# Kernel optimization log

Hardware: AMD Instinct MI355X
Metric: run time of the kernel (lower is better)

## Reference

```python
import jax, jax.numpy as jnp
import numpy as np

BATCH, D_IN, D_OUT = 2048, 1024, 4096


def setup_inputs() -> dict:
    key = jax.random.key(0)
    kx, kw = jax.random.split(key)
    x = jax.random.normal(kx, (BATCH, D_IN), dtype=jnp.float32)
    W = jax.random.normal(kw, (D_IN, D_OUT), dtype=jnp.float32)  # nn.Parameter init: N(0,1)
    return {"x": x, "W": W}


def reference(x, W):
    # out[b,o] = -1/2 * sum_i (x[b,i] - W[i,o])^2
    # instead of materializing the [B, O, I] broadcast tensor.
    x_sq = jnp.sum(x * x, axis=1, keepdims=True)          # [B, 1]
    w_sq = jnp.sum(W * W, axis=0, keepdims=True)          # [1, O]
    xw = jnp.matmul(x, W)                                  # [B, O] GEMM
    return -0.5 * (x_sq - 2.0 * xw + w_sq)
```

## Files before the change

### kernel.cpp

```cpp
#include <hip/hip_runtime.h>
#include <stdint.h>

#define BATCH 2048
#define DIN   1024
#define DOUT  4096


__device__ __forceinline__ ushort f2bf(float f) {
    uint32_t u = __float_as_uint(f);
    u += 0x7fffu + ((u >> 16) & 1u);
    return (ushort)(u >> 16);
}

__device__ __forceinline__ void async_copy16(const void* gsrc, void* ldst) {
    __builtin_amdgcn_global_load_lds(
        reinterpret_cast<uint32_t __attribute__((address_space(1)))*>(
            reinterpret_cast<uintptr_t>(gsrc)),
        reinterpret_cast<uint32_t __attribute__((address_space(3)))*>(
            reinterpret_cast<uintptr_t>(ldst)),
        16, 0, 0);
}

typedef __bf16 bf16x8 __attribute__((ext_vector_type(8)));
typedef float  f32x4  __attribute__((ext_vector_type(4)));

__global__ __launch_bounds__(256) void prep_fused(
    const float* __restrict__ x, const float* __restrict__ W,
    ushort* __restrict__ xb, ushort* __restrict__ wbt,
    float* __restrict__ xsq, float* __restrict__ wsq_part)
{
    __shared__ float smem[64 * 65 + 64];
    const int t = threadIdx.x;

    if (blockIdx.x < BATCH) {
        const int row = blockIdx.x;
        const float4 v = *(const float4*)(x + (size_t)row * DIN + t * 4);
        ushort4 pk;
        pk.x = f2bf(v.x); pk.y = f2bf(v.y); pk.z = f2bf(v.z); pk.w = f2bf(v.w);
        *(ushort4*)(xb + (size_t)row * DIN + t * 4) = pk;

        float s = v.x * v.x + v.y * v.y + v.z * v.z + v.w * v.w;
        #pragma unroll
        for (int off = 32; off > 0; off >>= 1) s += __shfl_down(s, off);
        if ((t & 63) == 0) smem[t >> 6] = s;
        __syncthreads();
        if (t == 0) xsq[row] = smem[0] + smem[1] + smem[2] + smem[3];
    } else {
        const int wblk = blockIdx.x - BATCH;
        const int o0 = (wblk & 63) * 64;
        const int i0 = (wblk >> 6) * 64;
        float (*tile)[65] = (float(*)[65])smem;
        float* csum = smem + 64 * 65;
        const int c4 = (t & 15) * 4;
        const int r0 = t >> 4;

        if (t < 64) csum[t] = 0.f;
        __syncthreads();

        float ss0 = 0.f, ss1 = 0.f, ss2 = 0.f, ss3 = 0.f;
        #pragma unroll
        for (int p = 0; p < 4; ++p) {
            const int r = r0 + p * 16;
            const float4 v = *(const float4*)&W[(size_t)(i0 + r) * DOUT + o0 + c4];
            tile[r][c4 + 0] = v.x; tile[r][c4 + 1] = v.y;
            tile[r][c4 + 2] = v.z; tile[r][c4 + 3] = v.w;
            ss0 += v.x * v.x; ss1 += v.y * v.y;
            ss2 += v.z * v.z; ss3 += v.w * v.w;
        }
        atomicAdd(&csum[c4 + 0], ss0);
        atomicAdd(&csum[c4 + 1], ss1);
        atomicAdd(&csum[c4 + 2], ss2);
        atomicAdd(&csum[c4 + 3], ss3);
        __syncthreads();
        if (t < 64) wsq_part[(size_t)(wblk >> 6) * DOUT + o0 + t] = csum[t];

        #pragma unroll
        for (int p = 0; p < 4; ++p) {
            const int orow = r0 + p * 16;
            ushort4 pk;
            pk.x = f2bf(tile[c4 + 0][orow]);
            pk.y = f2bf(tile[c4 + 1][orow]);
            pk.z = f2bf(tile[c4 + 2][orow]);
            pk.w = f2bf(tile[c4 + 3][orow]);
            *(ushort4*)&wbt[(size_t)(o0 + orow) * DIN + i0 + c4] = pk;
        }
    }
}

#define BM 128
#define BN 128
#define BK 64
#define NT (DIN / BK)

__global__ __launch_bounds__(256, 2) void gemm_epi(
    const ushort* __restrict__ A,
    const ushort* __restrict__ Bt,
    const float* __restrict__ xsq,
    const float* __restrict__ wsq_part,
    float* __restrict__ out)
{
    __shared__ __align__(16) ushort sA[2][BM * BK];
    __shared__ __align__(16) ushort sB[2][BN * BK];

    const int tid  = threadIdx.x;
    const int wv   = tid >> 6;
    const int lane = tid & 63;
    const int wr = wv >> 1, wc = wv & 1;

    const int bid = blockIdx.x;
    const int k = bid & 7, loc = bid >> 3;
    const int bx = (k & 3) * 8 + (loc & 7);
    const int by = (k >> 2) * 8 + (loc >> 3);
    const int m0 = by * BM;
    const int n0 = bx * BN;

    const int srow = tid >> 3;
    const int scol = (((tid & 7) ^ (srow & 7)) << 3);
    const ushort* ag = A  + (size_t)(m0 + srow) * DIN + scol;
    const ushort* bg = Bt + (size_t)(n0 + srow) * DIN + scol;

    const int fr  = lane & 15;
    const int q4  = lane >> 4;
    const int x7  = lane & 7;
    const int arow = wr * 64 + fr;
    const int brow = wc * 64 + fr;
    const int sl0 = ((q4)     ^ x7) << 3;
    const int sl1 = ((4 + q4) ^ x7) << 3;

    f32x4 acc[4][4] = {};

    auto stage = [&](int b, int kt) {
        ushort* da = &sA[b][0] + wv * 512;
        ushort* db = &sB[b][0] + wv * 512;
        #pragma unroll
        for (int q = 0; q < 4; ++q) {
            async_copy16(ag + (size_t)q * 32 * DIN + kt, da + q * 2048);
            async_copy16(bg + (size_t)q * 32 * DIN + kt, db + q * 2048);
        }
    };

    stage(0, 0);
    __syncthreads();
    int cur = 0;

    for (int t = 0; t < NT; ++t) {
        if (t + 1 < NT) stage(cur ^ 1, (t + 1) * BK);

        const ushort* pa = &sA[cur][0];
        const ushort* pb = &sB[cur][0];
        bf16x8 fa[2][4], fb[2][4];
        #pragma unroll
        for (int i = 0; i < 4; ++i) {
            fa[0][i] = *(const bf16x8*)&pa[(arow + i * 16) * BK + sl0];
            fa[1][i] = *(const bf16x8*)&pa[(arow + i * 16) * BK + sl1];
            fb[0][i] = *(const bf16x8*)&pb[(brow + i * 16) * BK + sl0];
            fb[1][i] = *(const bf16x8*)&pb[(brow + i * 16) * BK + sl1];
        }

        __builtin_amdgcn_s_setprio(1);
        #pragma unroll
        for (int ks = 0; ks < 2; ++ks)
            #pragma unroll
            for (int mi = 0; mi < 4; ++mi)
                #pragma unroll
                for (int ni = 0; ni < 4; ++ni)
                    acc[mi][ni] = __builtin_amdgcn_mfma_f32_16x16x32_bf16(
                        fa[ks][mi], fb[ks][ni], acc[mi][ni], 0, 0, 0);
        __builtin_amdgcn_s_setprio(0);

        __syncthreads();
        cur ^= 1;
    }

    const int er = q4 * 4;
    const int ec = fr;

    float wt[4];
    #pragma unroll
    for (int ni = 0; ni < 4; ++ni) {
        const int col = n0 + wc * 64 + ni * 16 + ec;
        float s = 0.f;
        #pragma unroll
        for (int j = 0; j < 16; ++j) s += wsq_part[(size_t)j * DOUT + col];
        wt[ni] = s;
    }

    #pragma unroll
    for (int mi = 0; mi < 4; ++mi) {
        const int row = m0 + wr * 64 + mi * 16 + er;
        #pragma unroll
        for (int ni = 0; ni < 4; ++ni) {
            const int col = n0 + wc * 64 + ni * 16 + ec;
            #pragma unroll
            for (int r = 0; r < 4; ++r) {
                out[(size_t)(row + r) * DOUT + col] =
                    acc[mi][ni][r] - 0.5f * (xsq[row + r] + wt[ni]);
            }
        }
    }
}


extern "C" void kernel_launch(void* const* d_in, const int* in_sizes, int n_in,
                              void* d_out, int out_size, void* d_ws, size_t ws_size,
                              hipStream_t stream) {
    const float* x = (const float*)d_in[0];
    const float* W = (const float*)d_in[1];
    float* out = (float*)d_out;

    char* ws = (char*)d_ws;
    ushort* xb  = (ushort*)ws;
    ushort* wbt = (ushort*)(ws + (4u << 20));
    float*  xsq = (float*)(ws + (12u << 20));
    float*  wsq_part = (float*)(ws + (12u << 20) + (16u << 10));

    prep_fused<<<BATCH + (DOUT / 64) * (DIN / 64), 256, 0, stream>>>(
        x, W, xb, wbt, xsq, wsq_part);
    gemm_epi<<<(DOUT / BN) * (BATCH / BM), 256, 0, stream>>>(
        xb, wbt, xsq, wsq_part, out);
}
```

Before: 105.0 us.

## Fuse prep and GEMM into one persistent kernel with a grid barrier

Merges the bf16 conversion/norm prep kernel and the GEMM-epilogue kernel into a single launch. Each of the 512 blocks processes six prep units, then all blocks synchronize through a global atomic counter before running the GEMM, with LDS shared via a union. This aims to remove the inter-kernel launch gap, but it adds a memset launch and a spin barrier that relies on all blocks being co-resident.

```diff
diff --git a/kernel.cpp b/kernel.cpp
--- a/kernel.cpp
+++ b/kernel.cpp
@@ -24,90 +24,98 @@
 typedef __bf16 bf16x8 __attribute__((ext_vector_type(8)));
 typedef float  f32x4  __attribute__((ext_vector_type(4)));
 
-__global__ __launch_bounds__(256) void prep_fused(
-    const float* __restrict__ x, const float* __restrict__ W,
-    ushort* __restrict__ xb, ushort* __restrict__ wbt,
-    float* __restrict__ xsq, float* __restrict__ wsq_part)
-{
-    __shared__ float smem[64 * 65 + 64];
-    const int t = threadIdx.x;
-
-    if (blockIdx.x < BATCH) {
-        const int row = blockIdx.x;
-        const float4 v = *(const float4*)(x + (size_t)row * DIN + t * 4);
-        ushort4 pk;
-        pk.x = f2bf(v.x); pk.y = f2bf(v.y); pk.z = f2bf(v.z); pk.w = f2bf(v.w);
-        *(ushort4*)(xb + (size_t)row * DIN + t * 4) = pk;
-
-        float s = v.x * v.x + v.y * v.y + v.z * v.z + v.w * v.w;
-        #pragma unroll
-        for (int off = 32; off > 0; off >>= 1) s += __shfl_down(s, off);
-        if ((t & 63) == 0) smem[t >> 6] = s;
-        __syncthreads();
-        if (t == 0) xsq[row] = smem[0] + smem[1] + smem[2] + smem[3];
-    } else {
-        const int wblk = blockIdx.x - BATCH;
-        const int o0 = (wblk & 63) * 64;
-        const int i0 = (wblk >> 6) * 64;
-        float (*tile)[65] = (float(*)[65])smem;
-        float* csum = smem + 64 * 65;
-        const int c4 = (t & 15) * 4;
-        const int r0 = t >> 4;
-
-        if (t < 64) csum[t] = 0.f;
-        __syncthreads();
-
-        float ss0 = 0.f, ss1 = 0.f, ss2 = 0.f, ss3 = 0.f;
-        #pragma unroll
-        for (int p = 0; p < 4; ++p) {
-            const int r = r0 + p * 16;
-            const float4 v = *(const float4*)&W[(size_t)(i0 + r) * DOUT + o0 + c4];
-            tile[r][c4 + 0] = v.x; tile[r][c4 + 1] = v.y;
-            tile[r][c4 + 2] = v.z; tile[r][c4 + 3] = v.w;
-            ss0 += v.x * v.x; ss1 += v.y * v.y;
-            ss2 += v.z * v.z; ss3 += v.w * v.w;
-        }
-        atomicAdd(&csum[c4 + 0], ss0);
-        atomicAdd(&csum[c4 + 1], ss1);
-        atomicAdd(&csum[c4 + 2], ss2);
-        atomicAdd(&csum[c4 + 3], ss3);
-        __syncthreads();
-        if (t < 64) wsq_part[(size_t)(wblk >> 6) * DOUT + o0 + t] = csum[t];
-
-        #pragma unroll
-        for (int p = 0; p < 4; ++p) {
-            const int orow = r0 + p * 16;
-            ushort4 pk;
-            pk.x = f2bf(tile[c4 + 0][orow]);
-            pk.y = f2bf(tile[c4 + 1][orow]);
-            pk.z = f2bf(tile[c4 + 2][orow]);
-            pk.w = f2bf(tile[c4 + 3][orow]);
-            *(ushort4*)&wbt[(size_t)(o0 + orow) * DIN + i0 + c4] = pk;
-        }
-    }
-}
-
 #define BM 128
 #define BN 128
 #define BK 64
 #define NT (DIN / BK)
-
-__global__ __launch_bounds__(256, 2) void gemm_epi(
-    const ushort* __restrict__ A,
-    const ushort* __restrict__ Bt,
-    const float* __restrict__ xsq,
-    const float* __restrict__ wsq_part,
+#define NBLK ((DOUT / BN) * (BATCH / BM))
+
+__global__ __launch_bounds__(256, 2) void fused_all(
+    const float* __restrict__ x, const float* __restrict__ W,
+    ushort* __restrict__ xb, ushort* __restrict__ wbt,
+    float* __restrict__ xsq, float* __restrict__ wsq_part,
+    unsigned int* __restrict__ bar,
     float* __restrict__ out)
 {
-    __shared__ __align__(16) ushort sA[2][BM * BK];
-    __shared__ __align__(16) ushort sB[2][BN * BK];
-
-    const int tid  = threadIdx.x;
+    __shared__ __align__(16) union {
+        struct { float tile[64][65]; float csum[64]; } w;
+        struct { ushort a[2][BM * BK]; ushort b[2][BN * BK]; } g;
+    } u;
+
+    const int tid = threadIdx.x;
+    const int bid = blockIdx.x;
+
+    for (int uu = 0; uu < 6; ++uu) {
+        const int unit = bid * 6 + uu;
+        if (uu) __syncthreads();
+        if (unit < BATCH) {
+            const int row = unit;
+            const float4 v = *(const float4*)(x + (size_t)row * DIN + tid * 4);
+            ushort4 pk;
+            pk.x = f2bf(v.x); pk.y = f2bf(v.y); pk.z = f2bf(v.z); pk.w = f2bf(v.w);
+            *(ushort4*)(xb + (size_t)row * DIN + tid * 4) = pk;
+
+            float s = v.x * v.x + v.y * v.y + v.z * v.z + v.w * v.w;
+            #pragma unroll
+            for (int off = 32; off > 0; off >>= 1) s += __shfl_down(s, off);
+            if ((tid & 63) == 0) u.w.csum[tid >> 6] = s;
+            __syncthreads();
+            if (tid == 0)
+                xsq[row] = u.w.csum[0] + u.w.csum[1] + u.w.csum[2] + u.w.csum[3];
+        } else {
+            const int wblk = unit - BATCH;
+            const int o0 = (wblk & 63) * 64;
+            const int i0 = (wblk >> 6) * 64;
+            const int c4 = (tid & 15) * 4;
+            const int r0 = tid >> 4;
+
+            if (tid < 64) u.w.csum[tid] = 0.f;
+            __syncthreads();
+
+            float ss0 = 0.f, ss1 = 0.f, ss2 = 0.f, ss3 = 0.f;
+            #pragma unroll
+            for (int p = 0; p < 4; ++p) {
+                const int r = r0 + p * 16;
+                const float4 v = *(const float4*)&W[(size_t)(i0 + r) * DOUT + o0 + c4];
+                u.w.tile[r][c4 + 0] = v.x; u.w.tile[r][c4 + 1] = v.y;
+                u.w.tile[r][c4 + 2] = v.z; u.w.tile[r][c4 + 3] = v.w;
+                ss0 += v.x * v.x; ss1 += v.y * v.y;
+                ss2 += v.z * v.z; ss3 += v.w * v.w;
+            }
+            atomicAdd(&u.w.csum[c4 + 0], ss0);
+            atomicAdd(&u.w.csum[c4 + 1], ss1);
+            atomicAdd(&u.w.csum[c4 + 2], ss2);
+            atomicAdd(&u.w.csum[c4 + 3], ss3);
+            __syncthreads();
+            if (tid < 64) wsq_part[(size_t)(wblk >> 6) * DOUT + o0 + tid] = u.w.csum[tid];
+
+            #pragma unroll
+            for (int p = 0; p < 4; ++p) {
+                const int orow = r0 + p * 16;
+                ushort4 pk;
+                pk.x = f2bf(u.w.tile[c4 + 0][orow]);
+                pk.y = f2bf(u.w.tile[c4 + 1][orow]);
+                pk.z = f2bf(u.w.tile[c4 + 2][orow]);
+                pk.w = f2bf(u.w.tile[c4 + 3][orow]);
+                *(ushort4*)&wbt[(size_t)(o0 + orow) * DIN + i0 + c4] = pk;
+            }
+        }
+    }
+
+    __threadfence();
+    __syncthreads();
+    if (tid == 0) {
+        __hip_atomic_fetch_add(bar, 1u, __ATOMIC_RELEASE, __HIP_MEMORY_SCOPE_AGENT);
+        while (__hip_atomic_load(bar, __ATOMIC_ACQUIRE, __HIP_MEMORY_SCOPE_AGENT)
+               < (unsigned int)NBLK)
+            __builtin_amdgcn_s_sleep(2);
+    }
+    __syncthreads();
+
     const int wv   = tid >> 6;
     const int lane = tid & 63;
     const int wr = wv >> 1, wc = wv & 1;
 
-    const int bid = blockIdx.x;
     const int k = bid & 7, loc = bid >> 3;
     const int bx = (k & 3) * 8 + (loc & 7);
     const int by = (k >> 2) * 8 + (loc >> 3);
@@ -116,8 +124,8 @@
 
     const int srow = tid >> 3;
     const int scol = (((tid & 7) ^ (srow & 7)) << 3);
-    const ushort* ag = A  + (size_t)(m0 + srow) * DIN + scol;
-    const ushort* bg = Bt + (size_t)(n0 + srow) * DIN + scol;
+    const ushort* ag = xb  + (size_t)(m0 + srow) * DIN + scol;
+    const ushort* bg = wbt + (size_t)(n0 + srow) * DIN + scol;
 
     const int fr  = lane & 15;
     const int q4  = lane >> 4;
@@ -129,9 +137,14 @@
 
     f32x4 acc[4][4] = {};
 
+    ushort* sA0 = &u.g.a[0][0];
+    ushort* sA1 = &u.g.a[1][0];
+    ushort* sB0 = &u.g.b[0][0];
+    ushort* sB1 = &u.g.b[1][0];
+
     auto stage = [&](int b, int kt) {
-        ushort* da = &sA[b][0] + wv * 512;
-        ushort* db = &sB[b][0] + wv * 512;
+        ushort* da = (b ? sA1 : sA0) + wv * 512;
+        ushort* db = (b ? sB1 : sB0) + wv * 512;
         #pragma unroll
         for (int q = 0; q < 4; ++q) {
             async_copy16(ag + (size_t)q * 32 * DIN + kt, da + q * 2048);
@@ -146,8 +159,8 @@
     for (int t = 0; t < NT; ++t) {
         if (t + 1 < NT) stage(cur ^ 1, (t + 1) * BK);
 
-        const ushort* pa = &sA[cur][0];
-        const ushort* pb = &sB[cur][0];
+        const ushort* pa = cur ? sA1 : sA0;
+        const ushort* pb = cur ? sB1 : sB0;
         bf16x8 fa[2][4], fb[2][4];
         #pragma unroll
         for (int i = 0; i < 4; ++i) {
@@ -213,9 +226,8 @@
     ushort* wbt = (ushort*)(ws + (4u << 20));
     float*  xsq = (float*)(ws + (12u << 20));
     float*  wsq_part = (float*)(ws + (12u << 20) + (16u << 10));
-
-    prep_fused<<<BATCH + (DOUT / 64) * (DIN / 64), 256, 0, stream>>>(
-        x, W, xb, wbt, xsq, wsq_part);
-    gemm_epi<<<(DOUT / BN) * (BATCH / BM), 256, 0, stream>>>(
-        xb, wbt, xsq, wsq_part, out);
-}
+    unsigned int* bar = (unsigned int*)(ws + (13u << 20));
+
+    hipMemsetAsync(bar, 0, sizeof(unsigned int), stream);
+    fused_all<<<NBLK, 256, 0, stream>>>(x, W, xb, wbt, xsq, wsq_part, bar, out);
+}
```

New measurement: 208.7 us. 98.7% more time.
